# Performance work log

Measured on AMD Instinct MI355X. Metric: run time of the kernel, lower is better.

## Reference

```python
import jax, jax.numpy as jnp
import numpy as np

N_NODES = 100000
N_EDGES = 1600000
F_IN = 128
HEADS = 4
C_OUT = 32
NEG_SLOPE = 0.2


def setup_inputs() -> dict:
    key = jax.random.key(0)
    k1, k2, k3, k4, k5, k6 = jax.random.split(key, 6)
    x = jax.random.normal(k1, (N_NODES, F_IN), dtype=jnp.float32)
    edge_index = jax.random.randint(k2, (2, N_EDGES), 0, N_NODES, dtype=jnp.int64)
    # glorot-ish scales
    W = jax.random.normal(k3, (F_IN, HEADS * C_OUT), dtype=jnp.float32) * (1.0 / np.sqrt(F_IN))
    att_src = jax.random.normal(k4, (HEADS, C_OUT), dtype=jnp.float32) * (1.0 / np.sqrt(C_OUT))
    att_dst = jax.random.normal(k5, (HEADS, C_OUT), dtype=jnp.float32) * (1.0 / np.sqrt(C_OUT))
    bias = jnp.zeros((HEADS * C_OUT,), dtype=jnp.float32)
    return {"x": x, "edge_index": edge_index, "W": W,
            "att_src": att_src, "att_dst": att_dst, "bias": bias}


def _gat_forward(x, edge_index, W, att_src, att_dst, bias):
    N = x.shape[0]
    H, C = att_src.shape
    h = (x @ W).reshape(N, H, C)                      # [N,H,C]
    # PyG GATConv default: add self-loops
    loops = jnp.arange(N, dtype=edge_index.dtype)
    src = jnp.concatenate([edge_index[0], loops])     # [E+N]
    dst = jnp.concatenate([edge_index[1], loops])
    a_src = jnp.einsum("nhc,hc->nh", h, att_src)      # [N,H]
    a_dst = jnp.einsum("nhc,hc->nh", h, att_dst)
    e = jax.nn.leaky_relu(a_src[src] + a_dst[dst], NEG_SLOPE)  # [E+N,H]
    # segment softmax over destination node (every node has a self-loop)
    m = jax.ops.segment_max(e, dst, num_segments=N)
    e = jnp.exp(e - m[dst])
    s = jax.ops.segment_sum(e, dst, num_segments=N)
    alpha = e / (s[dst] + 1e-16)                      # [E+N,H]
    msg = h[src] * alpha[:, :, None]                  # [E+N,H,C]
    out = jax.ops.segment_sum(msg, dst, num_segments=N).reshape(N, H * C)
    return jnp.tanh(out + bias)


def reference(x, edge_index, W, att_src, att_dst, bias):
    return _gat_forward(x, edge_index, W, att_src, att_dst, bias)
```

## Files before the change

### kernel.cpp

```cpp
#include <hip/hip_runtime.h>
#include <math.h>

#define NN 100000
#define NE 1600000
#define F_IN 128
#define HEADS 4
#define HC 128
#define NEG_SLOPE 0.2f
#define NBKT 391
#define BCAP 5120
#define LDK 136
#define NSTRIP 6250

typedef __attribute__((ext_vector_type(8))) short bf16x8;
typedef __attribute__((ext_vector_type(4))) float f32x4;

static __device__ __forceinline__ short f2bf_rne(float f) {
    unsigned u = __float_as_uint(f);
    unsigned r = (u + 0x7FFFu + ((u >> 16) & 1u)) >> 16;
    return (short)r;
}
static __device__ __forceinline__ float bf2f(short s) {
    return __uint_as_float(((unsigned)(unsigned short)s) << 16);
}

__global__ __launch_bounds__(256) void prep_kernel(
        const float* __restrict__ W, short* __restrict__ wt_hi, short* __restrict__ wt_lo,
        const int* __restrict__ ei, int* __restrict__ flag, int* __restrict__ bcur) {
    if (blockIdx.x == 0 && threadIdx.x < 64) {
        int l = threadIdx.x;
        int v = ei[2 * l + 1];
        for (int off = 1; off < 64; off <<= 1) v |= __shfl_xor(v, off);
        if (l == 0) *flag = (v == 0) ? 1 : 0;
    }
    if (blockIdx.x == 1 || blockIdx.x == 2) {
        int z = (blockIdx.x - 1) * 256 + threadIdx.x;
        if (z < NBKT) bcur[z] = 0;
    }
    int i = blockIdx.x * 256 + threadIdx.x;
    if (i >= F_IN * HC) return;
    int k = i >> 7, n = i & 127;
    float f = W[k * HC + n];
    short hb = f2bf_rne(f);
    wt_hi[n * F_IN + k] = hb;
    wt_lo[n * F_IN + k] = f2bf_rne(f - bf2f(hb));
}

__global__ __launch_bounds__(256, 4) void mfma_gemm_kernel(
        const float* __restrict__ x, const short* __restrict__ wt_hi,
        const short* __restrict__ wt_lo, const float* __restrict__ att_src,
        const float* __restrict__ att_dst, unsigned short* __restrict__ h_bf,
        float* __restrict__ a_src, float* __restrict__ a_dst) {
    __shared__ short lw_hi[64 * LDK];
    __shared__ short lw_lo[64 * LDK];
    int t = threadIdx.x;
    int blk = blockIdx.x;

    for (int c = t; c < 1024; c += 256) {
        int n = c >> 4;
        int kk = (c & 15) * 8;
        *(bf16x8*)(lw_hi + n * LDK + kk) = *(const bf16x8*)(wt_hi + n * F_IN + kk);
        *(bf16x8*)(lw_lo + n * LDK + kk) = *(const bf16x8*)(wt_lo + n * F_IN + kk);
    }
    __syncthreads();

    int strip = blk * 4 + (t >> 6);
    int valid = strip < NSTRIP;
    int sclamp = valid ? strip : NSTRIP - 1;
    int lane = t & 63;
    int l15 = lane & 15;
    int q = lane >> 4;

    f32x4 acc[8];
#pragma unroll
    for (int nt = 0; nt < 8; ++nt) acc[nt] = (f32x4){0.f, 0.f, 0.f, 0.f};

    bf16x8 ah[4], al[4];
    const float* xp = x + (size_t)(sclamp * 16 + l15) * F_IN + q * 8;

#pragma unroll
    for (int ki = 0; ki < 4; ++ki) {
        float4 v0 = *(const float4*)(xp + ki * 32);
        float4 v1 = *(const float4*)(xp + ki * 32 + 4);
        float vv[8] = {v0.x, v0.y, v0.z, v0.w, v1.x, v1.y, v1.z, v1.w};
#pragma unroll
        for (int j = 0; j < 8; ++j) {
            short hb = f2bf_rne(vv[j]);
            ah[ki][j] = hb;
            al[ki][j] = f2bf_rne(vv[j] - bf2f(hb));
        }
        int koff = ki * 32 + q * 8;
#pragma unroll
        for (int nt = 0; nt < 4; ++nt) {
            int lidx = (nt * 16 + l15) * LDK + koff;
            bf16x8 b_hi = *(const bf16x8*)(lw_hi + lidx);
            bf16x8 b_lo = *(const bf16x8*)(lw_lo + lidx);
            acc[nt] = __builtin_amdgcn_mfma_f32_16x16x32_bf16(ah[ki], b_hi, acc[nt], 0, 0, 0);
            acc[nt] = __builtin_amdgcn_mfma_f32_16x16x32_bf16(al[ki], b_hi, acc[nt], 0, 0, 0);
            acc[nt] = __builtin_amdgcn_mfma_f32_16x16x32_bf16(ah[ki], b_lo, acc[nt], 0, 0, 0);
        }
    }

    __syncthreads();
    for (int c = t; c < 1024; c += 256) {
        int n = c >> 4;
        int kk = (c & 15) * 8;
        *(bf16x8*)(lw_hi + n * LDK + kk) = *(const bf16x8*)(wt_hi + (64 + n) * F_IN + kk);
        *(bf16x8*)(lw_lo + n * LDK + kk) = *(const bf16x8*)(wt_lo + (64 + n) * F_IN + kk);
    }
    __syncthreads();

#pragma unroll
    for (int ki = 0; ki < 4; ++ki) {
        int koff = ki * 32 + q * 8;
#pragma unroll
        for (int nt = 0; nt < 4; ++nt) {
            int lidx = (nt * 16 + l15) * LDK + koff;
            bf16x8 b_hi = *(const bf16x8*)(lw_hi + lidx);
            bf16x8 b_lo = *(const bf16x8*)(lw_lo + lidx);
            acc[4 + nt] = __builtin_amdgcn_mfma_f32_16x16x32_bf16(ah[ki], b_hi, acc[4 + nt], 0, 0, 0);
            acc[4 + nt] = __builtin_amdgcn_mfma_f32_16x16x32_bf16(al[ki], b_hi, acc[4 + nt], 0, 0, 0);
            acc[4 + nt] = __builtin_amdgcn_mfma_f32_16x16x32_bf16(ah[ki], b_lo, acc[4 + nt], 0, 0, 0);
        }
    }

    if (!valid) return;

    int orow = strip * 16 + q * 4;
#pragma unroll
    for (int nt = 0; nt < 8; ++nt)
#pragma unroll
        for (int r = 0; r < 4; ++r)
            h_bf[(size_t)(orow + r) * HC + nt * 16 + l15] =
                (unsigned short)f2bf_rne(acc[nt][r]);

#pragma unroll
    for (int hd = 0; hd < 4; ++hd) {
        float as0 = att_src[hd * 32 + l15];
        float as1 = att_src[hd * 32 + 16 + l15];
        float ad0 = att_dst[hd * 32 + l15];
        float ad1 = att_dst[hd * 32 + 16 + l15];
#pragma unroll
        for (int r = 0; r < 4; ++r) {
            float ps = acc[2 * hd][r] * as0 + acc[2 * hd + 1][r] * as1;
            float pd = acc[2 * hd][r] * ad0 + acc[2 * hd + 1][r] * ad1;
#pragma unroll
            for (int off = 1; off < 16; off <<= 1) {
                ps += __shfl_xor(ps, off);
                pd += __shfl_xor(pd, off);
            }
            if (l15 == 0) {
                int row = orow + r;
                a_src[row * 4 + hd] = ps;
                a_dst[row * 4 + hd] = pd;
            }
        }
    }
}

__global__ __launch_bounds__(256) void bucket_scatter_kernel(
        const int* __restrict__ ei, const int* __restrict__ flag,
        int* __restrict__ bcur, unsigned* __restrict__ pairs) {
    __shared__ int lhist[NBKT];
    __shared__ int gbase[NBKT];
    int t = threadIdx.x;
    for (int i = t; i < NBKT; i += 256) lhist[i] = 0;
    __syncthreads();
    int is64 = *flag;
    int base = blockIdx.x * 4096;

    unsigned wrd[16];
    int meta[16];
#pragma unroll
    for (int it = 0; it < 16; ++it) {
        int e = base + it * 256 + t;
        if (e < NE) {
            int src = is64 ? ei[2 * e] : ei[e];
            int dst = is64 ? ei[2 * NE + 2 * e] : ei[NE + e];
            int b = dst >> 8;
            int r = atomicAdd(&lhist[b], 1);
            wrd[it] = (unsigned)src | ((unsigned)(dst & 255) << 17);
            meta[it] = b | (r << 9);
        } else {
            meta[it] = -1;
        }
    }
    __syncthreads();
    for (int i = t; i < NBKT; i += 256)
        gbase[i] = lhist[i] ? atomicAdd(&bcur[i], lhist[i]) : 0;
    __syncthreads();
#pragma unroll
    for (int it = 0; it < 16; ++it) {
        if (meta[it] >= 0) {
            int b = meta[it] & 511;
            int r = meta[it] >> 9;
            pairs[(size_t)b * BCAP + gbase[b] + r] = wrd[it];
        }
    }
}

__global__ __launch_bounds__(256) void bucket_csr_kernel(
        const int* __restrict__ bcur, const unsigned* __restrict__ pairs,
        const float* __restrict__ a_src, const float* __restrict__ a_dst,
        int* __restrict__ deg, int* __restrict__ offsets,
        int* __restrict__ csr_src, unsigned* __restrict__ wal) {
    __shared__ unsigned lpairs[BCAP];
    __shared__ int sd[256];
    __shared__ int cnt256[256];
    __shared__ int lcur[256];

    int b = blockIdx.x;
    int t = threadIdx.x;
    int node = (b << 8) + t;

    int partial = 0;
    for (int i = t; i < b; i += 256) partial += bcur[i];
    sd[t] = partial;
    __syncthreads();
    for (int off = 128; off > 0; off >>= 1) {
        if (t < off) sd[t] += sd[t + off];
        __syncthreads();
    }
    int bktbase = sd[0];
    __syncthreads();

    cnt256[t] = 0;
    __syncthreads();

    int cnt = bcur[b];
    const unsigned* __restrict__ bp = pairs + (size_t)b * BCAP;
    for (int i = t; i < cnt; i += 256) {
        unsigned w = bp[i];
        lpairs[i] = w;
        atomicAdd(&cnt256[w >> 17], 1);
    }
    __syncthreads();

    int v = cnt256[t];
    sd[t] = v;
    __syncthreads();
    for (int off = 1; off < 256; off <<= 1) {
        int u = (t >= off) ? sd[t - off] : 0;
        __syncthreads();
        sd[t] += u;
        __syncthreads();
    }
    int myoff = bktbase + sd[t] - v;
    if (node < NN) {
        deg[node] = v;
        offsets[node] = myoff;
    }
    lcur[t] = myoff;
    __syncthreads();

    for (int i = t; i < cnt; i += 256) {
        unsigned w = lpairs[i];
        int src = (int)(w & 0x1FFFFu);
        int dl = (int)(w >> 17);
        float4 as = ((const float4*)a_src)[src];
        float4 ad = ((const float4*)a_dst)[(b << 8) + dl];
        float e0 = as.x + ad.x; e0 = (e0 < 0.f) ? NEG_SLOPE * e0 : e0;
        float e1 = as.y + ad.y; e1 = (e1 < 0.f) ? NEG_SLOPE * e1 : e1;
        float e2 = as.z + ad.z; e2 = (e2 < 0.f) ? NEG_SLOPE * e2 : e2;
        float e3 = as.w + ad.w; e3 = (e3 < 0.f) ? NEG_SLOPE * e3 : e3;
        float w0 = __expf(e0), w1 = __expf(e1), w2 = __expf(e2), w3 = __expf(e3);
        int pos = atomicAdd(&lcur[dl], 1);
        csr_src[pos] = src;
        unsigned lo = (unsigned)(unsigned short)f2bf_rne(w0) |
                      ((unsigned)(unsigned short)f2bf_rne(w1) << 16);
        unsigned hi = (unsigned)(unsigned short)f2bf_rne(w2) |
                      ((unsigned)(unsigned short)f2bf_rne(w3) << 16);
        ((uint2*)wal)[pos] = make_uint2(lo, hi);
    }
}

__global__ __launch_bounds__(256) void gat_aggr_kernel(
        const int* __restrict__ offsets, const int* __restrict__ deg,
        const int* __restrict__ csr_src, const unsigned* __restrict__ wal,
        const float* __restrict__ a_src, const float* __restrict__ a_dst,
        const unsigned* __restrict__ h2, const float* __restrict__ bias,
        float* __restrict__ out) {
    int wid = (blockIdx.x * 256 + threadIdx.x) >> 6;
    int dst = __builtin_amdgcn_readfirstlane(wid);
    if (dst >= NN) return;
    int lane = threadIdx.x & 63;
    int hd = lane >> 4;
    unsigned hsel2 = (unsigned)(hd & 2);
    unsigned hsel1 = (unsigned)(hd & 1);

    int start = offsets[dst];
    int n = deg[dst];

    float accx = 0.f, accy = 0.f, wsum = 0.f;
    int j = 0;
    for (; j + 7 < n; j += 8) {
        int base = start + j;
        int s0 = csr_src[base + 0];
        int s1 = csr_src[base + 1];
        int s2 = csr_src[base + 2];
        int s3 = csr_src[base + 3];
        int s4 = csr_src[base + 4];
        int s5 = csr_src[base + 5];
        int s6 = csr_src[base + 6];
        int s7 = csr_src[base + 7];
        uint2 wv0 = ((const uint2*)wal)[base + 0];
        uint2 wv1 = ((const uint2*)wal)[base + 1];
        uint2 wv2 = ((const uint2*)wal)[base + 2];
        uint2 wv3 = ((const uint2*)wal)[base + 3];
        uint2 wv4 = ((const uint2*)wal)[base + 4];
        uint2 wv5 = ((const uint2*)wal)[base + 5];
        uint2 wv6 = ((const uint2*)wal)[base + 6];
        uint2 wv7 = ((const uint2*)wal)[base + 7];
        unsigned u0 = h2[(size_t)s0 * 64 + lane];
        unsigned u1 = h2[(size_t)s1 * 64 + lane];
        unsigned u2 = h2[(size_t)s2 * 64 + lane];
        unsigned u3 = h2[(size_t)s3 * 64 + lane];
        unsigned u4 = h2[(size_t)s4 * 64 + lane];
        unsigned u5 = h2[(size_t)s5 * 64 + lane];
        unsigned u6 = h2[(size_t)s6 * 64 + lane];
        unsigned u7 = h2[(size_t)s7 * 64 + lane];
        unsigned ws0 = hsel2 ? wv0.y : wv0.x;
        unsigned ws1 = hsel2 ? wv1.y : wv1.x;
        unsigned ws2 = hsel2 ? wv2.y : wv2.x;
        unsigned ws3 = hsel2 ? wv3.y : wv3.x;
        unsigned ws4 = hsel2 ? wv4.y : wv4.x;
        unsigned ws5 = hsel2 ? wv5.y : wv5.x;
        unsigned ws6 = hsel2 ? wv6.y : wv6.x;
        unsigned ws7 = hsel2 ? wv7.y : wv7.x;
        float w0 = __uint_as_float(hsel1 ? (ws0 & 0xFFFF0000u) : (ws0 << 16));
        float w1 = __uint_as_float(hsel1 ? (ws1 & 0xFFFF0000u) : (ws1 << 16));
        float w2 = __uint_as_float(hsel1 ? (ws2 & 0xFFFF0000u) : (ws2 << 16));
        float w3 = __uint_as_float(hsel1 ? (ws3 & 0xFFFF0000u) : (ws3 << 16));
        float w4 = __uint_as_float(hsel1 ? (ws4 & 0xFFFF0000u) : (ws4 << 16));
        float w5 = __uint_as_float(hsel1 ? (ws5 & 0xFFFF0000u) : (ws5 << 16));
        float w6 = __uint_as_float(hsel1 ? (ws6 & 0xFFFF0000u) : (ws6 << 16));
        float w7 = __uint_as_float(hsel1 ? (ws7 & 0xFFFF0000u) : (ws7 << 16));
        wsum += ((w0 + w1) + (w2 + w3)) + ((w4 + w5) + (w6 + w7));
        accx += w0 * __uint_as_float(u0 << 16);
        accy += w0 * __uint_as_float(u0 & 0xFFFF0000u);
        accx += w1 * __uint_as_float(u1 << 16);
        accy += w1 * __uint_as_float(u1 & 0xFFFF0000u);
        accx += w2 * __uint_as_float(u2 << 16);
        accy += w2 * __uint_as_float(u2 & 0xFFFF0000u);
        accx += w3 * __uint_as_float(u3 << 16);
        accy += w3 * __uint_as_float(u3 & 0xFFFF0000u);
        accx += w4 * __uint_as_float(u4 << 16);
        accy += w4 * __uint_as_float(u4 & 0xFFFF0000u);
        accx += w5 * __uint_as_float(u5 << 16);
        accy += w5 * __uint_as_float(u5 & 0xFFFF0000u);
        accx += w6 * __uint_as_float(u6 << 16);
        accy += w6 * __uint_as_float(u6 & 0xFFFF0000u);
        accx += w7 * __uint_as_float(u7 << 16);
        accy += w7 * __uint_as_float(u7 & 0xFFFF0000u);
    }
    for (; j + 3 < n; j += 4) {
        int base = start + j;
        int s0 = csr_src[base + 0];
        int s1 = csr_src[base + 1];
        int s2 = csr_src[base + 2];
        int s3 = csr_src[base + 3];
        uint2 wv0 = ((const uint2*)wal)[base + 0];
        uint2 wv1 = ((const uint2*)wal)[base + 1];
        uint2 wv2 = ((const uint2*)wal)[base + 2];
        uint2 wv3 = ((const uint2*)wal)[base + 3];
        unsigned u0 = h2[(size_t)s0 * 64 + lane];
        unsigned u1 = h2[(size_t)s1 * 64 + lane];
        unsigned u2 = h2[(size_t)s2 * 64 + lane];
        unsigned u3 = h2[(size_t)s3 * 64 + lane];
        unsigned ws0 = hsel2 ? wv0.y : wv0.x;
        unsigned ws1 = hsel2 ? wv1.y : wv1.x;
        unsigned ws2 = hsel2 ? wv2.y : wv2.x;
        unsigned ws3 = hsel2 ? wv3.y : wv3.x;
        float w0 = __uint_as_float(hsel1 ? (ws0 & 0xFFFF0000u) : (ws0 << 16));
        float w1 = __uint_as_float(hsel1 ? (ws1 & 0xFFFF0000u) : (ws1 << 16));
        float w2 = __uint_as_float(hsel1 ? (ws2 & 0xFFFF0000u) : (ws2 << 16));
        float w3 = __uint_as_float(hsel1 ? (ws3 & 0xFFFF0000u) : (ws3 << 16));
        wsum += (w0 + w1) + (w2 + w3);
        accx += w0 * __uint_as_float(u0 << 16);
        accy += w0 * __uint_as_float(u0 & 0xFFFF0000u);
        accx += w1 * __uint_as_float(u1 << 16);
        accy += w1 * __uint_as_float(u1 & 0xFFFF0000u);
        accx += w2 * __uint_as_float(u2 << 16);
        accy += w2 * __uint_as_float(u2 & 0xFFFF0000u);
        accx += w3 * __uint_as_float(u3 << 16);
        accy += w3 * __uint_as_float(u3 & 0xFFFF0000u);
    }
    for (; j < n; ++j) {
        int base = start + j;
        int s0 = csr_src[base];
        uint2 wv0 = ((const uint2*)wal)[base];
        unsigned u0 = h2[(size_t)s0 * 64 + lane];
        unsigned ws0 = hsel2 ? wv0.y : wv0.x;
        float w0 = __uint_as_float(hsel1 ? (ws0 & 0xFFFF0000u) : (ws0 << 16));
        wsum += w0;
        accx += w0 * __uint_as_float(u0 << 16);
        accy += w0 * __uint_as_float(u0 & 0xFFFF0000u);
    }

    float e = a_src[dst * 4 + hd] + a_dst[dst * 4 + hd];
    e = (e < 0.f) ? NEG_SLOPE * e : e;
    float sf = __expf(e);
    float inv = 1.f / (wsum + sf + 1e-16f);

    unsigned us = h2[(size_t)dst * 64 + lane];
    float2 b2 = ((const float2*)bias)[lane];
    float ox = tanhf((accx + sf * __uint_as_float(us << 16)) * inv + b2.x);
    float oy = tanhf((accy + sf * __uint_as_float(us & 0xFFFF0000u)) * inv + b2.y);
    ((float2*)out)[(size_t)dst * 64 + lane] = make_float2(ox, oy);
}

extern "C" void kernel_launch(void* const* d_in, const int* in_sizes, int n_in,
                              void* d_out, int out_size, void* d_ws, size_t ws_size,
                              hipStream_t stream) {
    const float* x       = (const float*)d_in[0];
    const int*   ei      = (const int*)  d_in[1];
    const float* W       = (const float*)d_in[2];
    const float* att_src = (const float*)d_in[3];
    const float* att_dst = (const float*)d_in[4];
    const float* bias    = (const float*)d_in[5];
    float* out = (float*)d_out;

    unsigned short* h_bf = (unsigned short*)d_ws;
    float* a_src = (float*)(h_bf + (size_t)NN * HC);
    float* a_dst = a_src + (size_t)NN * HEADS;
    short* wt_hi = (short*)(a_dst + (size_t)NN * HEADS);
    short* wt_lo = wt_hi + F_IN * HC;
    int* flag    = (int*)(wt_lo + F_IN * HC);
    int* bcur    = flag + 4;
    int* deg     = bcur + NBKT + 1;
    int* offsets = deg + NN;
    int* csr_src = offsets + NN;
    unsigned* wal = (unsigned*)(csr_src + NE);
    unsigned* pairs = (unsigned*)(wal + (size_t)NE * 2);

    hipLaunchKernelGGL(prep_kernel, dim3(64), dim3(256), 0, stream,
                       W, wt_hi, wt_lo, ei, flag, bcur);

    hipLaunchKernelGGL(bucket_scatter_kernel, dim3((NE + 4095) / 4096), dim3(256), 0, stream,
                       ei, flag, bcur, pairs);

    hipLaunchKernelGGL(mfma_gemm_kernel, dim3(1563), dim3(256), 0, stream,
                       x, wt_hi, wt_lo, att_src, att_dst, h_bf, a_src, a_dst);

    hipLaunchKernelGGL(bucket_csr_kernel, dim3(NBKT), dim3(256), 0, stream,
                       bcur, pairs, a_src, a_dst, deg, offsets, csr_src, wal);

    hipLaunchKernelGGL(gat_aggr_kernel, dim3(NN * 64 / 256), dim3(256), 0, stream,
                       offsets, deg, csr_src, wal, a_src, a_dst,
                       (const unsigned*)h_bf, bias, out);
}
```

Measured before the change: 258.9 us.

## Fuse bucket scatter into GEMM launch and use packed FMA in aggregation

Merges the edge bucket-scatter kernel into the MFMA GEMM kernel as extra leading blocks that share a union of shared memory, so the two independent stages run concurrently in one launch. The bcur zeroing moves from prep_kernel to a hipMemsetAsync. The aggregation inner loop now processes edges in pairs with v_pk_fma_f32/v_pk_add_f32 inline asm and branchless weight extraction, which cuts VALU instruction count. The changes add a memset launch and inline-asm dependencies, and the fused kernel's launch bounds now also apply to the scatter blocks.

Result: no change. 263.5 us (+1.8%).

```diff
diff --git a/kernel.cpp b/kernel.cpp
--- a/kernel.cpp
+++ b/kernel.cpp
@@ -8,12 +8,14 @@
 #define HC 128
 #define NEG_SLOPE 0.2f
 #define NBKT 391
+#define NSCAT 391
 #define BCAP 5120
 #define LDK 136
 #define NSTRIP 6250
 
 typedef __attribute__((ext_vector_type(8))) short bf16x8;
 typedef __attribute__((ext_vector_type(4))) float f32x4;
+typedef __attribute__((ext_vector_type(2))) float f32x2;
 
 static __device__ __forceinline__ short f2bf_rne(float f) {
     unsigned u = __float_as_uint(f);
@@ -24,18 +26,26 @@
     return __uint_as_float(((unsigned)(unsigned short)s) << 16);
 }
 
+static __device__ __forceinline__ void pk_fma(f32x2& d, f32x2 a, f32x2 b) {
+    asm("v_pk_fma_f32 %0, %1, %2, %0 op_sel:[0,0,0] op_sel_hi:[1,1,1]"
+        : "+v"(d) : "v"(a), "v"(b));
+}
+static __device__ __forceinline__ void pk_add(f32x2& d, f32x2 a) {
+    asm("v_pk_add_f32 %0, %1, %0 op_sel:[0,0] op_sel_hi:[1,1]"
+        : "+v"(d) : "v"(a));
+}
+static __device__ __forceinline__ f32x2 mkpair(float a, float b) {
+    f32x2 r; r.x = a; r.y = b; return r;
+}
+
 __global__ __launch_bounds__(256) void prep_kernel(
         const float* __restrict__ W, short* __restrict__ wt_hi, short* __restrict__ wt_lo,
-        const int* __restrict__ ei, int* __restrict__ flag, int* __restrict__ bcur) {
+        const int* __restrict__ ei, int* __restrict__ flag) {
     if (blockIdx.x == 0 && threadIdx.x < 64) {
         int l = threadIdx.x;
         int v = ei[2 * l + 1];
         for (int off = 1; off < 64; off <<= 1) v |= __shfl_xor(v, off);
         if (l == 0) *flag = (v == 0) ? 1 : 0;
-    }
-    if (blockIdx.x == 1 || blockIdx.x == 2) {
-        int z = (blockIdx.x - 1) * 256 + threadIdx.x;
-        if (z < NBKT) bcur[z] = 0;
     }
     int i = blockIdx.x * 256 + threadIdx.x;
     if (i >= F_IN * HC) return;
@@ -46,21 +56,63 @@
     wt_lo[n * F_IN + k] = f2bf_rne(f - bf2f(hb));
 }
 
-__global__ __launch_bounds__(256, 4) void mfma_gemm_kernel(
+__global__ __launch_bounds__(256, 4) void fused_gemm_scatter_kernel(
         const float* __restrict__ x, const short* __restrict__ wt_hi,
         const short* __restrict__ wt_lo, const float* __restrict__ att_src,
         const float* __restrict__ att_dst, unsigned short* __restrict__ h_bf,
-        float* __restrict__ a_src, float* __restrict__ a_dst) {
-    __shared__ short lw_hi[64 * LDK];
-    __shared__ short lw_lo[64 * LDK];
+        float* __restrict__ a_src, float* __restrict__ a_dst,
+        const int* __restrict__ ei, const int* __restrict__ flag,
+        int* __restrict__ bcur, unsigned* __restrict__ pairs) {
+    __shared__ union SM {
+        struct { short hi[64 * LDK]; short lo[64 * LDK]; } w;
+        struct { int lhist[NBKT]; int gbase[NBKT]; } b;
+    } sm;
     int t = threadIdx.x;
-    int blk = blockIdx.x;
+
+    if (blockIdx.x < NSCAT) {
+        for (int i = t; i < NBKT; i += 256) sm.b.lhist[i] = 0;
+        __syncthreads();
+        int is64 = *flag;
+        int base = blockIdx.x * 4096;
+
+        unsigned wrd[16];
+        int meta[16];
+#pragma unroll
+        for (int it = 0; it < 16; ++it) {
+            int e = base + it * 256 + t;
+            if (e < NE) {
+                int src = is64 ? ei[2 * e] : ei[e];
+                int dst = is64 ? ei[2 * NE + 2 * e] : ei[NE + e];
+                int b = dst >> 8;
+                int r = atomicAdd(&sm.b.lhist[b], 1);
+                wrd[it] = (unsigned)src | ((unsigned)(dst & 255) << 17);
+                meta[it] = b | (r << 9);
+            } else {
+                meta[it] = -1;
+            }
+        }
+        __syncthreads();
+        for (int i = t; i < NBKT; i += 256)
+            sm.b.gbase[i] = sm.b.lhist[i] ? atomicAdd(&bcur[i], sm.b.lhist[i]) : 0;
+        __syncthreads();
+#pragma unroll
+        for (int it = 0; it < 16; ++it) {
+            if (meta[it] >= 0) {
+                int b = meta[it] & 511;
+                int r = meta[it] >> 9;
+                pairs[(size_t)b * BCAP + sm.b.gbase[b] + r] = wrd[it];
+            }
+        }
+        return;
+    }
+
+    int blk = blockIdx.x - NSCAT;
 
     for (int c = t; c < 1024; c += 256) {
         int n = c >> 4;
         int kk = (c & 15) * 8;
-        *(bf16x8*)(lw_hi + n * LDK + kk) = *(const bf16x8*)(wt_hi + n * F_IN + kk);
-        *(bf16x8*)(lw_lo + n * LDK + kk) = *(const bf16x8*)(wt_lo + n * F_IN + kk);
+        *(bf16x8*)(sm.w.hi + n * LDK + kk) = *(const bf16x8*)(wt_hi + n * F_IN + kk);
+        *(bf16x8*)(sm.w.lo + n * LDK + kk) = *(const bf16x8*)(wt_lo + n * F_IN + kk);
     }
     __syncthreads();
 
@@ -93,8 +145,8 @@
 #pragma unroll
         for (int nt = 0; nt < 4; ++nt) {
             int lidx = (nt * 16 + l15) * LDK + koff;
-            bf16x8 b_hi = *(const bf16x8*)(lw_hi + lidx);
-            bf16x8 b_lo = *(const bf16x8*)(lw_lo + lidx);
+            bf16x8 b_hi = *(const bf16x8*)(sm.w.hi + lidx);
+            bf16x8 b_lo = *(const bf16x8*)(sm.w.lo + lidx);
             acc[nt] = __builtin_amdgcn_mfma_f32_16x16x32_bf16(ah[ki], b_hi, acc[nt], 0, 0, 0);
             acc[nt] = __builtin_amdgcn_mfma_f32_16x16x32_bf16(al[ki], b_hi, acc[nt], 0, 0, 0);
             acc[nt] = __builtin_amdgcn_mfma_f32_16x16x32_bf16(ah[ki], b_lo, acc[nt], 0, 0, 0);
@@ -105,8 +157,8 @@
     for (int c = t; c < 1024; c += 256) {
         int n = c >> 4;
         int kk = (c & 15) * 8;
-        *(bf16x8*)(lw_hi + n * LDK + kk) = *(const bf16x8*)(wt_hi + (64 + n) * F_IN + kk);
-        *(bf16x8*)(lw_lo + n * LDK + kk) = *(const bf16x8*)(wt_lo + (64 + n) * F_IN + kk);
+        *(bf16x8*)(sm.w.hi + n * LDK + kk) = *(const bf16x8*)(wt_hi + (64 + n) * F_IN + kk);
+        *(bf16x8*)(sm.w.lo + n * LDK + kk) = *(const bf16x8*)(wt_lo + (64 + n) * F_IN + kk);
     }
     __syncthreads();
 
@@ -116,8 +168,8 @@
 #pragma unroll
         for (int nt = 0; nt < 4; ++nt) {
             int lidx = (nt * 16 + l15) * LDK + koff;
-            bf16x8 b_hi = *(const bf16x8*)(lw_hi + lidx);
-            bf16x8 b_lo = *(const bf16x8*)(lw_lo + lidx);
+            bf16x8 b_hi = *(const bf16x8*)(sm.w.hi + lidx);
+            bf16x8 b_lo = *(const bf16x8*)(sm.w.lo + lidx);
             acc[4 + nt] = __builtin_amdgcn_mfma_f32_16x16x32_bf16(ah[ki], b_hi, acc[4 + nt], 0, 0, 0);
             acc[4 + nt] = __builtin_amdgcn_mfma_f32_16x16x32_bf16(al[ki], b_hi, acc[4 + nt], 0, 0, 0);
             acc[4 + nt] = __builtin_amdgcn_mfma_f32_16x16x32_bf16(ah[ki], b_lo, acc[4 + nt], 0, 0, 0);
@@ -154,47 +206,6 @@
                 a_src[row * 4 + hd] = ps;
                 a_dst[row * 4 + hd] = pd;
             }
-        }
-    }
-}
-
-__global__ __launch_bounds__(256) void bucket_scatter_kernel(
-        const int* __restrict__ ei, const int* __restrict__ flag,
-        int* __restrict__ bcur, unsigned* __restrict__ pairs) {
-    __shared__ int lhist[NBKT];
-    __shared__ int gbase[NBKT];
-    int t = threadIdx.x;
-    for (int i = t; i < NBKT; i += 256) lhist[i] = 0;
-    __syncthreads();
-    int is64 = *flag;
-    int base = blockIdx.x * 4096;
-
-    unsigned wrd[16];
-    int meta[16];
-#pragma unroll
-    for (int it = 0; it < 16; ++it) {
-        int e = base + it * 256 + t;
-        if (e < NE) {
-            int src = is64 ? ei[2 * e] : ei[e];
-            int dst = is64 ? ei[2 * NE + 2 * e] : ei[NE + e];
-            int b = dst >> 8;
-            int r = atomicAdd(&lhist[b], 1);
-            wrd[it] = (unsigned)src | ((unsigned)(dst & 255) << 17);
-            meta[it] = b | (r << 9);
-        } else {
-            meta[it] = -1;
-        }
-    }
-    __syncthreads();
-    for (int i = t; i < NBKT; i += 256)
-        gbase[i] = lhist[i] ? atomicAdd(&bcur[i], lhist[i]) : 0;
-    __syncthreads();
-#pragma unroll
-    for (int it = 0; it < 16; ++it) {
-        if (meta[it] >= 0) {
-            int b = meta[it] & 511;
-            int r = meta[it] >> 9;
-            pairs[(size_t)b * BCAP + gbase[b] + r] = wrd[it];
         }
     }
 }
@@ -286,12 +297,13 @@
     int lane = threadIdx.x & 63;
     int hd = lane >> 4;
     unsigned hsel2 = (unsigned)(hd & 2);
-    unsigned hsel1 = (unsigned)(hd & 1);
+    unsigned shamt = (hd & 1) ? 0u : 16u;
 
     int start = offsets[dst];
     int n = deg[dst];
 
-    float accx = 0.f, accy = 0.f, wsum = 0.f;
+    f32x2 accx2 = {0.f, 0.f}, accy2 = {0.f, 0.f}, ws2 = {0.f, 0.f};
+
     int j = 0;
     for (; j + 7 < n; j += 8) {
         int base = start + j;
@@ -319,79 +331,46 @@
         unsigned u5 = h2[(size_t)s5 * 64 + lane];
         unsigned u6 = h2[(size_t)s6 * 64 + lane];
         unsigned u7 = h2[(size_t)s7 * 64 + lane];
-        unsigned ws0 = hsel2 ? wv0.y : wv0.x;
-        unsigned ws1 = hsel2 ? wv1.y : wv1.x;
-        unsigned ws2 = hsel2 ? wv2.y : wv2.x;
-        unsigned ws3 = hsel2 ? wv3.y : wv3.x;
-        unsigned ws4 = hsel2 ? wv4.y : wv4.x;
-        unsigned ws5 = hsel2 ? wv5.y : wv5.x;
-        unsigned ws6 = hsel2 ? wv6.y : wv6.x;
-        unsigned ws7 = hsel2 ? wv7.y : wv7.x;
-        float w0 = __uint_as_float(hsel1 ? (ws0 & 0xFFFF0000u) : (ws0 << 16));
-        float w1 = __uint_as_float(hsel1 ? (ws1 & 0xFFFF0000u) : (ws1 << 16));
-        float w2 = __uint_as_float(hsel1 ? (ws2 & 0xFFFF0000u) : (ws2 << 16));
-        float w3 = __uint_as_float(hsel1 ? (ws3 & 0xFFFF0000u) : (ws3 << 16));
-        float w4 = __uint_as_float(hsel1 ? (ws4 & 0xFFFF0000u) : (ws4 << 16));
-        float w5 = __uint_as_float(hsel1 ? (ws5 & 0xFFFF0000u) : (ws5 << 16));
-        float w6 = __uint_as_float(hsel1 ? (ws6 & 0xFFFF0000u) : (ws6 << 16));
-        float w7 = __uint_as_float(hsel1 ? (ws7 & 0xFFFF0000u) : (ws7 << 16));
-        wsum += ((w0 + w1) + (w2 + w3)) + ((w4 + w5) + (w6 + w7));
-        accx += w0 * __uint_as_float(u0 << 16);
-        accy += w0 * __uint_as_float(u0 & 0xFFFF0000u);
-        accx += w1 * __uint_as_float(u1 << 16);
-        accy += w1 * __uint_as_float(u1 & 0xFFFF0000u);
-        accx += w2 * __uint_as_float(u2 << 16);
-        accy += w2 * __uint_as_float(u2 & 0xFFFF0000u);
-        accx += w3 * __uint_as_float(u3 << 16);
-        accy += w3 * __uint_as_float(u3 & 0xFFFF0000u);
-        accx += w4 * __uint_as_float(u4 << 16);
-        accy += w4 * __uint_as_float(u4 & 0xFFFF0000u);
-        accx += w5 * __uint_as_float(u5 << 16);
-        accy += w5 * __uint_as_float(u5 & 0xFFFF0000u);
-        accx += w6 * __uint_as_float(u6 << 16);
-        accy += w6 * __uint_as_float(u6 & 0xFFFF0000u);
-        accx += w7 * __uint_as_float(u7 << 16);
-        accy += w7 * __uint_as_float(u7 & 0xFFFF0000u);
-    }
-    for (; j + 3 < n; j += 4) {
+#define EDGEPAIR(ua, ub, wva, wvb)                                              \
+        {                                                                       \
+            unsigned wsa = hsel2 ? wva.y : wva.x;                               \
+            unsigned wsb = hsel2 ? wvb.y : wvb.x;                               \
+            f32x2 wp = mkpair(__uint_as_float((wsa << shamt) & 0xFFFF0000u),    \
+                              __uint_as_float((wsb << shamt) & 0xFFFF0000u));   \
+            f32x2 hx = mkpair(__uint_as_float(ua << 16),                        \
+                              __uint_as_float(ub << 16));                       \
+            f32x2 hy = mkpair(__uint_as_float(ua & 0xFFFF0000u),                \
+                              __uint_as_float(ub & 0xFFFF0000u));               \
+            pk_add(ws2, wp);                                                    \
+            pk_fma(accx2, wp, hx);                                              \
+            pk_fma(accy2, wp, hy);                                              \
+        }
+        EDGEPAIR(u0, u1, wv0, wv1)
+        EDGEPAIR(u2, u3, wv2, wv3)
+        EDGEPAIR(u4, u5, wv4, wv5)
+        EDGEPAIR(u6, u7, wv6, wv7)
+    }
+    for (; j + 1 < n; j += 2) {
         int base = start + j;
         int s0 = csr_src[base + 0];
         int s1 = csr_src[base + 1];
-        int s2 = csr_src[base + 2];
-        int s3 = csr_src[base + 3];
         uint2 wv0 = ((const uint2*)wal)[base + 0];
         uint2 wv1 = ((const uint2*)wal)[base + 1];
-        uint2 wv2 = ((const uint2*)wal)[base + 2];
-        uint2 wv3 = ((const uint2*)wal)[base + 3];
         unsigned u0 = h2[(size_t)s0 * 64 + lane];
         unsigned u1 = h2[(size_t)s1 * 64 + lane];
-        unsigned u2 = h2[(size_t)s2 * 64 + lane];
-        unsigned u3 = h2[(size_t)s3 * 64 + lane];
-        unsigned ws0 = hsel2 ? wv0.y : wv0.x;
-        unsigned ws1 = hsel2 ? wv1.y : wv1.x;
-        unsigned ws2 = hsel2 ? wv2.y : wv2.x;
-        unsigned ws3 = hsel2 ? wv3.y : wv3.x;
-        float w0 = __uint_as_float(hsel1 ? (ws0 & 0xFFFF0000u) : (ws0 << 16));
-        float w1 = __uint_as_float(hsel1 ? (ws1 & 0xFFFF0000u) : (ws1 << 16));
-        float w2 = __uint_as_float(hsel1 ? (ws2 & 0xFFFF0000u) : (ws2 << 16));
-        float w3 = __uint_as_float(hsel1 ? (ws3 & 0xFFFF0000u) : (ws3 << 16));
-        wsum += (w0 + w1) + (w2 + w3);
-        accx += w0 * __uint_as_float(u0 << 16);
-        accy += w0 * __uint_as_float(u0 & 0xFFFF0000u);
-        accx += w1 * __uint_as_float(u1 << 16);
-        accy += w1 * __uint_as_float(u1 & 0xFFFF0000u);
-        accx += w2 * __uint_as_float(u2 << 16);
-        accy += w2 * __uint_as_float(u2 & 0xFFFF0000u);
-        accx += w3 * __uint_as_float(u3 << 16);
-        accy += w3 * __uint_as_float(u3 & 0xFFFF0000u);
-    }
-    for (; j < n; ++j) {
+        EDGEPAIR(u0, u1, wv0, wv1)
+    }
+#undef EDGEPAIR
+    float accx = accx2.x + accx2.y;
+    float accy = accy2.x + accy2.y;
+    float wsum = ws2.x + ws2.y;
+    if (j < n) {
         int base = start + j;
         int s0 = csr_src[base];
         uint2 wv0 = ((const uint2*)wal)[base];
         unsigned u0 = h2[(size_t)s0 * 64 + lane];
         unsigned ws0 = hsel2 ? wv0.y : wv0.x;
-        float w0 = __uint_as_float(hsel1 ? (ws0 & 0xFFFF0000u) : (ws0 << 16));
+        float w0 = __uint_as_float((ws0 << shamt) & 0xFFFF0000u);
         wsum += w0;
         accx += w0 * __uint_as_float(u0 << 16);
         accy += w0 * __uint_as_float(u0 & 0xFFFF0000u);
@@ -433,14 +412,14 @@
     unsigned* wal = (unsigned*)(csr_src + NE);
     unsigned* pairs = (unsigned*)(wal + (size_t)NE * 2);
 
+    hipMemsetAsync(bcur, 0, NBKT * sizeof(int), stream);
+
     hipLaunchKernelGGL(prep_kernel, dim3(64), dim3(256), 0, stream,
-                       W, wt_hi, wt_lo, ei, flag, bcur);
-
-    hipLaunchKernelGGL(bucket_scatter_kernel, dim3((NE + 4095) / 4096), dim3(256), 0, stream,
+                       W, wt_hi, wt_lo, ei, flag);
+
+    hipLaunchKernelGGL(fused_gemm_scatter_kernel, dim3(NSCAT + 1563), dim3(256), 0, stream,
+                       x, wt_hi, wt_lo, att_src, att_dst, h_bf, a_src, a_dst,
                        ei, flag, bcur, pairs);
-
-    hipLaunchKernelGGL(mfma_gemm_kernel, dim3(1563), dim3(256), 0, stream,
-                       x, wt_hi, wt_lo, att_src, att_dst, h_bf, a_src, a_dst);
 
     hipLaunchKernelGGL(bucket_csr_kernel, dim3(NBKT), dim3(256), 0, stream,
                        bcur, pairs, a_src, a_dst, deg, offsets, csr_src, wal);
```
